# Kernel optimization log

Measured on AMD Instinct MI355X. Metric: run time of the kernel, lower is better.

## Reference

```python
import jax, jax.numpy as jnp
import numpy as np
from jax import lax

EPS = 1e-8
SLOPE = 0.2

def _modconv(x, wv, W, b, sW, sB, demodulate, pad):
    # StyleGAN2 modulated conv, expressed in the equivalent fused form:
    # scale input by per-sample style s, shared-weight conv, then demodulate output.
    s = wv @ sW.T + sB                                   # [B, Cin]
    y = lax.conv_general_dilated(
        x * s[:, :, None, None], W, (1, 1), [(pad, pad), (pad, pad)],
        dimension_numbers=("NCHW", "OIHW", "NCHW"))      # [B, Cout, H, W]
    if demodulate:
        # d[b,o] = 1/sqrt(sum_{i,k,k} (W[o,i,k,k]*s[b,i])^2 + eps)
        d = lax.rsqrt(jnp.einsum("oihw,bi->bo", W * W, s * s) + EPS)
        y = y * d[:, :, None, None]
    return y + b[None, :, None, None]

def _up2(x):
    B, C, H, W = x.shape
    # matches torch F.interpolate(scale_factor=2, mode='bilinear', align_corners=False)
    return jax.image.resize(x, (B, C, 2 * H, 2 * W), method="bilinear")

def setup_inputs() -> dict:
    B, CIN, COUT, NZ, H = 8, 512, 512, 512, 32
    key = jax.random.key(0)
    ks = jax.random.split(key, 20)
    wscale3 = 1.0 / np.sqrt(CIN * 9)   # kaiming-ish equalized-lr scale baked into weights
    wscale1 = 1.0 / np.sqrt(COUT)
    sscale = 1.0 / np.sqrt(NZ)
    return {
        "maps": jax.random.normal(ks[0], (B, CIN, H, H), jnp.float32),
        "w": jax.random.normal(ks[1], (B, NZ), jnp.float32),
        "rgb": jax.random.normal(ks[2], (B, 3, H, H), jnp.float32),
        "noise0": jax.random.normal(ks[3], (B, 1, 2 * H, 2 * H), jnp.float32),
        "noise1": jax.random.normal(ks[4], (B, 1, 2 * H, 2 * H), jnp.float32),
        "w0": jax.random.normal(ks[5], (COUT, CIN, 3, 3), jnp.float32) * wscale3,
        "b0": jnp.zeros((COUT,), jnp.float32),
        "sW0": jax.random.normal(ks[6], (CIN, NZ), jnp.float32) * sscale,
        "sB0": jnp.ones((CIN,), jnp.float32),
        "ns0": jax.random.normal(ks[7], (COUT,), jnp.float32) * 0.1,
        "w1": jax.random.normal(ks[8], (COUT, COUT, 3, 3), jnp.float32) * wscale3,
        "b1": jnp.zeros((COUT,), jnp.float32),
        "sW1": jax.random.normal(ks[9], (COUT, NZ), jnp.float32) * sscale,
        "sB1": jnp.ones((COUT,), jnp.float32),
        "ns1": jax.random.normal(ks[10], (COUT,), jnp.float32) * 0.1,
        "rgbW": jax.random.normal(ks[11], (3, COUT, 1, 1), jnp.float32) * wscale1,
        "rgbB": jnp.zeros((3,), jnp.float32),
        "rgbSW": jax.random.normal(ks[12], (COUT, NZ), jnp.float32) * sscale,
        "rgbSB": jnp.ones((COUT,), jnp.float32),
    }

def reference(maps, w, rgb, noise0, noise1,
              w0, b0, sW0, sB0, ns0,
              w1, b1, sW1, sB1, ns1,
              rgbW, rgbB, rgbSW, rgbSB):
    rgb = _up2(rgb)
    x = _up2(maps)
    # layer 0: modulated conv 3x3 + noise + leakyrelu
    x = _modconv(x, w, w0, b0, sW0, sB0, True, 1)
    x = x + ns0[None, :, None, None] * noise0
    x = jnp.where(x >= 0, x, SLOPE * x)
    # layer 1
    x = _modconv(x, w, w1, b1, sW1, sB1, True, 1)
    x = x + ns1[None, :, None, None] * noise1
    x = jnp.where(x >= 0, x, SLOPE * x)
    # to_rgb: modulated 1x1 conv, no demodulation
    rgb_out = rgb + _modconv(x, w, rgbW, rgbB, rgbSW, rgbSB, False, 0)
    return (rgb_out, x)
```

## Files before the change

kernel.cpp:

```cpp
#include <hip/hip_runtime.h>

typedef unsigned short u16;
typedef short bf16x8 __attribute__((ext_vector_type(8)));
typedef float f32x4 __attribute__((ext_vector_type(4)));
typedef u16 u16x4 __attribute__((ext_vector_type(4)));
typedef u16 u16x8 __attribute__((ext_vector_type(8)));
typedef unsigned u32x4 __attribute__((ext_vector_type(4)));

__device__ __forceinline__ float b2f(u16 v) {
  union { unsigned u; float f; } x; x.u = ((unsigned)v) << 16; return x.f;
}
__device__ __forceinline__ u16 f2b(float f) {
  unsigned u = __float_as_uint(f);
  unsigned r = (u + 0x7FFFu + ((u >> 16) & 1u)) >> 16;
  return (u16)r;
}
__device__ __forceinline__ float rin(const void* p, size_t i, int bf) {
  return bf ? b2f(((const u16*)p)[i]) : ((const float*)p)[i];
}
__device__ __forceinline__ void async16(const void* g, void* l) {
  __builtin_amdgcn_global_load_lds((const __attribute__((address_space(1))) unsigned*)g,
                                   (__attribute__((address_space(3))) unsigned*)l, 16, 0, 0);
}
__device__ __forceinline__ int detect_bf(const unsigned* __restrict__ w0raw, int tid, int* shflag) {
  if (tid < 64) {
    const unsigned lo = w0raw[tid] & 0xFFFFu;
    const unsigned e = (lo >> 7) & 0xFFu;
    const unsigned long long bad = __ballot(e < 100u || e > 126u);
    if (tid == 0) *shflag = (bad == 0ull) ? 1 : 0;
  }
  __syncthreads();
  return *shflag;
}

__global__ void styleall_kernel(const void* __restrict__ w,
                                const void* __restrict__ sW0, const void* __restrict__ sB0,
                                const void* __restrict__ sW1, const void* __restrict__ sB1,
                                const void* __restrict__ sWR, const void* __restrict__ sBR,
                                float* __restrict__ s0, float* __restrict__ s1,
                                float* __restrict__ sR, const unsigned* __restrict__ w0raw) {
  __shared__ int shflag;
  const int tid = threadIdx.x;
  const int bf = detect_bf(w0raw, tid, &shflag);
  const int mat = blockIdx.z, b = blockIdx.y, oc = blockIdx.x;
  const void* sW = (mat == 0) ? sW0 : ((mat == 1) ? sW1 : sWR);
  const void* sB = (mat == 0) ? sB0 : ((mat == 1) ? sB1 : sBR);
  float* out = (mat == 0) ? s0 : ((mat == 1) ? s1 : sR);
  const int i = oc * 64 + (tid >> 2), q = tid & 3;
  float acc = 0.f;
  if (bf) {
    const u16* rp = (const u16*)sW + (size_t)i * 512 + q * 128;
    const u16* wp = (const u16*)w + b * 512 + q * 128;
    for (int z = 0; z < 128; z += 8) {
      u16x8 a = *(const u16x8*)(rp + z), c = *(const u16x8*)(wp + z);
#pragma unroll
      for (int j = 0; j < 8; ++j) acc += b2f(a[j]) * b2f(c[j]);
    }
  } else {
    const float* rp = (const float*)sW + (size_t)i * 512 + q * 128;
    const float* wp = (const float*)w + b * 512 + q * 128;
    for (int z = 0; z < 128; z += 4) {
      f32x4 a = *(const f32x4*)(rp + z), c = *(const f32x4*)(wp + z);
#pragma unroll
      for (int j = 0; j < 4; ++j) acc += a[j] * c[j];
    }
  }
  acc += __shfl_xor(acc, 1, 64);
  acc += __shfl_xor(acc, 2, 64);
  if (q == 0) out[b * 512 + i] = acc + rin(sB, i, bf);
}

__global__ void demod_kernel(const void* __restrict__ W0, const void* __restrict__ W1,
                             const float* __restrict__ s0, const float* __restrict__ s1,
                             float* __restrict__ dm0, float* __restrict__ dm1,
                             u16* __restrict__ Wp0, u16* __restrict__ Wp1,
                             const unsigned* __restrict__ w0raw) {
  __shared__ int shflag;
  __shared__ float wl[4608];
  __shared__ float wsq[512];
  const int tid = threadIdx.x, lane = tid & 63, wv = tid >> 6;
  const int bf = detect_bf(w0raw, tid, &shflag);
  const int o = blockIdx.x, layer = blockIdx.y;
  const void* W = layer ? W1 : W0;
  const float* s = layer ? s1 : s0;
  float* d = layer ? dm1 : dm0;
  u16* Wp = layer ? Wp1 : Wp0;

  if (bf) {
    const u16* src = (const u16*)W + (size_t)o * 4608;
    for (int e = tid; e < 576; e += 256) {
      u16x8 v = *(const u16x8*)(src + e * 8);
#pragma unroll
      for (int j = 0; j < 8; ++j) wl[e * 8 + j] = b2f(v[j]);
    }
  } else {
    const float* src = (const float*)W + (size_t)o * 4608;
    for (int e = tid; e < 1152; e += 256) {
      f32x4 v = *(const f32x4*)(src + e * 4);
#pragma unroll
      for (int j = 0; j < 4; ++j) wl[e * 4 + j] = v[j];
    }
  }
  __syncthreads();
  for (int i = tid; i < 512; i += 256) {
    float ss = 0.f;
#pragma unroll
    for (int t = 0; t < 9; ++t) {
      const float f = wl[i * 9 + t];
      ss += f * f;
      Wp[t * 262144 + o * 512 + i] = f2b(f);
    }
    wsq[i] = ss;
  }
  __syncthreads();
#pragma unroll
  for (int bb = 0; bb < 2; ++bb) {
    const int b = wv * 2 + bb;
    float part = 0.f;
    for (int i = lane; i < 512; i += 64) { const float sv = s[b * 512 + i]; part += wsq[i] * sv * sv; }
#pragma unroll
    for (int st = 1; st < 64; st <<= 1) part += __shfl_xor(part, st, 64);
    if (lane == 0) d[b * 512 + o] = rsqrtf(part + 1e-8f);
  }
}

__global__ void prep_kernel(u16* __restrict__ actB, u32x4* __restrict__ zr, int NB) {
  const int id = blockIdx.x, tid = threadIdx.x;
  if (id < NB * 65) {
    const int bl = id / 65, sub = id - bl * 65;
    const int c = sub * 256 + tid;
    const int px = c >> 6, seg = c & 63;
    int oy, ox;
    if (px < 66)       { oy = 0;  ox = px; }
    else if (px < 132) { oy = 65; ox = px - 66; }
    else { const int e = px - 132; oy = 1 + (e >> 1); ox = (e & 1) * 65; }
    u32x4 z = {0, 0, 0, 0};
    *(u32x4*)&actB[((size_t)(bl * 4356) + oy * 66 + ox) * 512 + seg * 8] = z;
  } else {
    const int c = (id - NB * 65) * 256 + tid;
    if (c < 24832) { u32x4 z = {0, 0, 0, 0}; zr[c] = z; }
  }
}

__global__ void upsample_kernel(const void* __restrict__ maps, const float* __restrict__ s,
                                void* __restrict__ outb, int b_base,
                                const unsigned* __restrict__ w0raw) {
  __shared__ int shflag;
  __shared__ float it[32][2][33];
  const int tid = threadIdx.x;
  const int bf = detect_bf(w0raw, tid, &shflag);
  const size_t esz = bf ? 2 : 4;
  u16* xg = (u16*)((char*)outb + (98304 + (size_t)(b_base >> 2) * 8388608) * esz);
  const int oy = blockIdx.x;
  const int i0 = blockIdx.y * 32;
  const int bl = blockIdx.z;
  const int bg = b_base + bl;
  const int m = oy >> 1;
  int iy0, iy1; float wy0, wy1;
  if ((oy & 1) == 0) { iy0 = (m > 0) ? m - 1 : 0; iy1 = m; wy0 = 0.25f; wy1 = 0.75f; }
  else               { iy0 = m; iy1 = (m < 31) ? m + 1 : 31; wy0 = 0.75f; wy1 = 0.25f; }
#pragma unroll
  for (int k = 0; k < 8; ++k) {
    const int e = tid + k * 256;
    const int c = e >> 6, wsel = (e >> 5) & 1, x = e & 31;
    const int iy = wsel ? iy1 : iy0;
    it[c][wsel][x] = rin(maps, ((size_t)(bg * 512 + i0 + c) * 32 + iy) * 32 + x, bf);
  }
  __syncthreads();
#pragma unroll
  for (int k = 0; k < 8; ++k) {
    const int e = tid + k * 256;
    const int xx = e >> 5, c = e & 31;
    const int mx = xx >> 1;
    int ix0, ix1; float wx0, wx1;
    if ((xx & 1) == 0) { ix0 = (mx > 0) ? mx - 1 : 0; ix1 = mx; wx0 = 0.25f; wx1 = 0.75f; }
    else               { ix0 = mx; ix1 = (mx < 31) ? mx + 1 : 31; wx0 = 0.75f; wx1 = 0.25f; }
    const float r0 = wx0 * it[c][0][ix0] + wx1 * it[c][0][ix1];
    const float r1 = wx0 * it[c][1][ix0] + wx1 * it[c][1][ix1];
    const float v = (wy0 * r0 + wy1 * r1) * s[bg * 512 + i0 + c];
    xg[((size_t)(bl * 4096) + oy * 64 + xx) * 512 + i0 + c] = f2b(v);
  }
}

template <int L>
__global__ __launch_bounds__(512) void conv_kernel(
    void* __restrict__ outb, u16* __restrict__ actBp,
    const u16* __restrict__ Wp, const float* __restrict__ dmod,
    const void* __restrict__ bias, const void* __restrict__ nsc,
    const void* __restrict__ noise, const float* __restrict__ saux,
    const u16* __restrict__ zbuf, const void* __restrict__ rgbW,
    float* __restrict__ rgbacc, int b_base,
    const unsigned* __restrict__ w0raw) {
  __shared__ __attribute__((aligned(16))) u16 lds[65536];
  __shared__ float rgbWl[L == 1 ? 1536 : 4];
  __shared__ int shflag;
  const int tid = threadIdx.x, lane = tid & 63, w = tid >> 6;
  const int bf = detect_bf(w0raw, tid, &shflag);
  const size_t esz = bf ? 2 : 4;

  const int lin = blockIdx.x + (blockIdx.y << 4) + (blockIdx.z << 5);
  const int cpx = (int)(gridDim.z << 2);
  const int wg = (lin & 7) * cpx + (lin >> 3);
  const int bl = wg >> 5, rem = wg & 31;
  const int o0 = (rem >> 4) << 8, n0 = (rem & 15) << 8;
  const int bg = b_base + bl;
  const int wm = w >> 2, wn = w & 3;

  if constexpr (L == 1) {
    for (int e = tid; e < 1536; e += 512) rgbWl[e] = rin(rgbW, e, bf);
  }
  const u16* xg = (const u16*)((const char*)outb +
                  (98304 + (size_t)(b_base >> 2) * 8388608) * esz);

  const int q = lane >> 4, m15 = lane & 15;
  const int lro = m15 * 64 + ((q ^ (lane & 7)) * 8);
  const int srow8 = lane >> 3, schunk = (lane & 7) ^ srow8;
  const size_t aAst = (size_t)(o0 + srow8) * 512 + schunk * 8;

  const int ka0 = (w < 4) ? (2 * w) : (16 + 2 * (w - 4));
  const int ka1 = ka0 + 8;
  const int kbe = (w & 3) * 8 + (w >> 2) * 2;
  const int kb0 = kbe, kb1 = kbe + 1, kb2 = kbe + 4, kb3 = kbe + 5;
  size_t pB[4]; int oyv[4], oxv[4];
  {
    const int kk4[4] = {kb0, kb1, kb2, kb3};
#pragma unroll
    for (int j = 0; j < 4; ++j) {
      const int p = n0 + kk4[j] * 8 + srow8;
      const int oy = p >> 6, ox = p & 63;
      oyv[j] = oy; oxv[j] = ox;
      pB[j] = ((size_t)bl * 4356 + oy * 66 + ox) * 512 + schunk * 8;
    }
  }

#define STAGE_A(k_, aoff_) \
  async16(Wp + (aoff_) + (size_t)(k_) * 4096, &lds[nbb + (k_) * 512])
#define STAGE_B(j_, k_, sb_, ty1_, tx1_, ko_) do {                                   \
    if constexpr (L == 0) {                                                          \
      const int iy_ = oyv[j_] + (ty1_), ix_ = oxv[j_] + (tx1_);                      \
      const u16* s_ = (((unsigned)iy_ < 64u) & ((unsigned)ix_ < 64u))                \
        ? (xg + ((size_t)((bl << 12) + (iy_ << 6) + ix_) * 512 + (ko_) + schunk * 8))\
        : (zbuf + schunk * 8);                                                       \
      async16(s_, &lds[nbb + 16384 + (k_) * 512]);                                   \
    } else {                                                                         \
      async16(actBp + pB[j_] + (size_t)(sb_), &lds[nbb + 16384 + (k_) * 512]);       \
    } } while (0)

  f32x4 acc[8][4] = {};
  {
    const int nbb = 0;
    const size_t aoff = aAst;
    STAGE_A(ka0, aoff); STAGE_A(ka0 + 1, aoff);
    STAGE_A(ka1, aoff); STAGE_A(ka1 + 1, aoff);
    STAGE_B(0, kb0, 0, -1, -1, 0);
    STAGE_B(1, kb1, 0, -1, -1, 0);
    STAGE_B(2, kb2, 0, -1, -1, 0);
    STAGE_B(3, kb3, 0, -1, -1, 0);
  }
  asm volatile("s_waitcnt vmcnt(0)" ::: "memory");
  __builtin_amdgcn_s_barrier();

  bf16x8 afr[4][2], bfA[2][2], bfB[2][2];
#pragma unroll 1
  for (int s = 0; s < 72; ++s) {
    const int db = s & 1;
    const int dbb = db << 15, nbb = dbb ^ 32768;
    const int s1 = s + 1, ok = (s1 < 72);
    const int tn = s1 >> 3, kon = (s1 & 7) << 6;
    const int tyn = (tn * 11) >> 5, txn = tn - tyn * 3;
    const size_t aoffn = (size_t)tn * 262144 + kon + aAst;
    const int sbn = (tyn * 66 + txn) * 512 + kon;
    const int ty1 = tyn - 1, tx1 = txn - 1;
    const int abase = dbb + wm * 8192;
    const int bbase = dbb + 16384 + wn * 4096;

#pragma unroll
    for (int mi = 0; mi < 4; ++mi) {
      afr[mi][0] = *(const bf16x8*)&lds[abase + mi * 1024 + lro];
      afr[mi][1] = *(const bf16x8*)&lds[abase + mi * 1024 + (lro ^ 32)];
    }
#pragma unroll
    for (int ni = 0; ni < 2; ++ni) {
      bfA[ni][0] = *(const bf16x8*)&lds[bbase + ni * 1024 + lro];
      bfA[ni][1] = *(const bf16x8*)&lds[bbase + ni * 1024 + (lro ^ 32)];
    }
    if (ok) { STAGE_A(ka0, aoffn); STAGE_A(ka0 + 1, aoffn); }
    __builtin_amdgcn_s_setprio(1);
#pragma unroll
    for (int mi = 0; mi < 4; ++mi)
#pragma unroll
      for (int ni = 0; ni < 2; ++ni)
#pragma unroll
        for (int kk = 0; kk < 2; ++kk)
          acc[mi][ni] = __builtin_amdgcn_mfma_f32_16x16x32_bf16(
              afr[mi][kk], bfA[ni][kk], acc[mi][ni], 0, 0, 0);
    __builtin_amdgcn_s_setprio(0);
    if (ok) { asm volatile("s_waitcnt vmcnt(4)" ::: "memory"); }
    else    { asm volatile("s_waitcnt vmcnt(2)" ::: "memory"); }
    __builtin_amdgcn_s_barrier();

#pragma unroll
    for (int ni = 0; ni < 2; ++ni) {
      bfB[ni][0] = *(const bf16x8*)&lds[bbase + 2048 + ni * 1024 + lro];
      bfB[ni][1] = *(const bf16x8*)&lds[bbase + 2048 + ni * 1024 + (lro ^ 32)];
    }
    if (ok) { STAGE_B(0, kb0, sbn, ty1, tx1, kon); STAGE_B(1, kb1, sbn, ty1, tx1, kon); }
    __builtin_amdgcn_s_setprio(1);
#pragma unroll
    for (int mi = 0; mi < 4; ++mi)
#pragma unroll
      for (int ni = 0; ni < 2; ++ni)
#pragma unroll
        for (int kk = 0; kk < 2; ++kk)
          acc[mi][2 + ni] = __builtin_amdgcn_mfma_f32_16x16x32_bf16(
              afr[mi][kk], bfB[ni][kk], acc[mi][2 + ni], 0, 0, 0);
    __builtin_amdgcn_s_setprio(0);
    if (ok) { asm volatile("s_waitcnt vmcnt(4)" ::: "memory"); }
    else    { asm volatile("s_waitcnt vmcnt(0)" ::: "memory"); }
    __builtin_amdgcn_s_barrier();

#pragma unroll
    for (int mi = 0; mi < 4; ++mi) {
      afr[mi][0] = *(const bf16x8*)&lds[abase + 4096 + mi * 1024 + lro];
      afr[mi][1] = *(const bf16x8*)&lds[abase + 4096 + mi * 1024 + (lro ^ 32)];
    }
    if (ok) { STAGE_B(2, kb2, sbn, ty1, tx1, kon); STAGE_B(3, kb3, sbn, ty1, tx1, kon); }
    __builtin_amdgcn_s_setprio(1);
#pragma unroll
    for (int mi = 0; mi < 4; ++mi)
#pragma unroll
      for (int ni = 0; ni < 2; ++ni)
#pragma unroll
        for (int kk = 0; kk < 2; ++kk)
          acc[4 + mi][ni] = __builtin_amdgcn_mfma_f32_16x16x32_bf16(
              afr[mi][kk], bfA[ni][kk], acc[4 + mi][ni], 0, 0, 0);
    __builtin_amdgcn_s_setprio(0);

    if (ok) { STAGE_A(ka1, aoffn); STAGE_A(ka1 + 1, aoffn); }
    __builtin_amdgcn_s_setprio(1);
#pragma unroll
    for (int mi = 0; mi < 4; ++mi)
#pragma unroll
      for (int ni = 0; ni < 2; ++ni)
#pragma unroll
        for (int kk = 0; kk < 2; ++kk)
          acc[4 + mi][2 + ni] = __builtin_amdgcn_mfma_f32_16x16x32_bf16(
              afr[mi][kk], bfB[ni][kk], acc[4 + mi][2 + ni], 0, 0, 0);
    __builtin_amdgcn_s_setprio(0);
    asm volatile("s_waitcnt vmcnt(4)" ::: "memory");
    __builtin_amdgcn_s_barrier();
  }
#undef STAGE_A
#undef STAGE_B

  if constexpr (L == 0) {
#pragma unroll
    for (int ai = 0; ai < 8; ++ai) {
      const int o = o0 + wm * 128 + ai * 16 + q * 4;
      const f32x4 dv = *(const f32x4*)&dmod[bg * 512 + o];
      const f32x4 sv = *(const f32x4*)&saux[bg * 512 + o];
      float bv[4], nv[4];
#pragma unroll
      for (int r = 0; r < 4; ++r) { bv[r] = rin(bias, o + r, bf); nv[r] = rin(nsc, o + r, bf); }
#pragma unroll
      for (int bj = 0; bj < 4; ++bj) {
        const int p = n0 + wn * 64 + bj * 16 + m15;
        const float np = rin(noise, (size_t)bg * 4096 + p, bf);
        u16x4 pack;
#pragma unroll
        for (int r = 0; r < 4; ++r) {
          float v = acc[ai][bj][r] * dv[r] + bv[r] + nv[r] * np;
          v = (v >= 0.f) ? v : 0.2f * v;
          pack[r] = f2b(v * sv[r]);
        }
        const int oy = p >> 6, ox = p & 63;
        *(u16x4*)&actBp[((size_t)(bl * 4356) + (oy + 1) * 66 + (ox + 1)) * 512 + o] = pack;
      }
    }
  } else {
    char* xreg = (char*)outb + 98304 * esz;
    float racc[4][3] = {};
#pragma unroll
    for (int ai = 0; ai < 8; ++ai) {
      const int o = o0 + wm * 128 + ai * 16 + q * 4;
      const f32x4 dv = *(const f32x4*)&dmod[bg * 512 + o];
      const f32x4 srv = *(const f32x4*)&saux[bg * 512 + o];
      float bv[4], nv[4], w0l[4], w1l[4], w2l[4];
#pragma unroll
      for (int r = 0; r < 4; ++r) {
        bv[r] = rin(bias, o + r, bf); nv[r] = rin(nsc, o + r, bf);
        w0l[r] = rgbWl[o + r]; w1l[r] = rgbWl[512 + o + r]; w2l[r] = rgbWl[1024 + o + r];
      }
#pragma unroll
      for (int bj = 0; bj < 4; ++bj) {
        const int p = n0 + wn * 64 + bj * 16 + m15;
        const float np = rin(noise, (size_t)bg * 4096 + p, bf);
#pragma unroll
        for (int r = 0; r < 4; ++r) {
          float v = acc[ai][bj][r] * dv[r] + bv[r] + nv[r] * np;
          v = (v >= 0.f) ? v : 0.2f * v;
          const size_t xi = (size_t)(bg * 512 + o + r) * 4096 + p;
          if (bf) ((u16*)xreg)[xi] = f2b(v); else ((float*)xreg)[xi] = v;
          const float xr = v * srv[r];
          racc[bj][0] += w0l[r] * xr;
          racc[bj][1] += w1l[r] * xr;
          racc[bj][2] += w2l[r] * xr;
        }
      }
    }
#pragma unroll
    for (int bj = 0; bj < 4; ++bj) {
      const int p = n0 + wn * 64 + bj * 16 + m15;
#pragma unroll
      for (int c = 0; c < 3; ++c) {
        float t = racc[bj][c];
        t += __shfl_xor(t, 16, 64);
        t += __shfl_xor(t, 32, 64);
        if (lane < 16) atomicAdd(&rgbacc[(size_t)(bg * 3 + c) * 4096 + p], t);
      }
    }
  }
}

__global__ void rgbfin_kernel(const float* __restrict__ rgbacc, const void* __restrict__ rgbB,
                              const void* __restrict__ rgb, void* __restrict__ outb,
                              const unsigned* __restrict__ w0raw) {
  __shared__ int shflag;
  const int tid = threadIdx.x;
  const int bf = detect_bf(w0raw, tid, &shflag);
  const int g = blockIdx.x * 256 + tid;
  const int b = g >> 12, p = g & 4095;
  const int oy = p >> 6, ox = p & 63;
  const int m = oy >> 1; int iy0, iy1; float wy0, wy1;
  if ((oy & 1) == 0) { iy0 = (m > 0) ? m - 1 : 0; iy1 = m; wy0 = 0.25f; wy1 = 0.75f; }
  else               { iy0 = m; iy1 = (m < 31) ? m + 1 : 31; wy0 = 0.75f; wy1 = 0.25f; }
  const int mx = ox >> 1; int ix0, ix1; float wx0, wx1;
  if ((ox & 1) == 0) { ix0 = (mx > 0) ? mx - 1 : 0; ix1 = mx; wx0 = 0.25f; wx1 = 0.75f; }
  else               { ix0 = mx; ix1 = (mx < 31) ? mx + 1 : 31; wx0 = 0.75f; wx1 = 0.25f; }
#pragma unroll
  for (int c = 0; c < 3; ++c) {
    const size_t rb = (size_t)(b * 3 + c) * 1024;
    const float up = wy0 * (wx0 * rin(rgb, rb + iy0 * 32 + ix0, bf) + wx1 * rin(rgb, rb + iy0 * 32 + ix1, bf))
                   + wy1 * (wx0 * rin(rgb, rb + iy1 * 32 + ix0, bf) + wx1 * rin(rgb, rb + iy1 * 32 + ix1, bf));
    const float v = up + rin(rgbB, c, bf) + rgbacc[(size_t)(b * 3 + c) * 4096 + p];
    const size_t oi = ((size_t)(b * 3 + c) << 12) + p;
    if (bf) ((u16*)outb)[oi] = f2b(v); else ((float*)outb)[oi] = v;
  }
}


extern "C" void kernel_launch(void* const* d_in, const int* in_sizes, int n_in,
                              void* d_out, int out_size, void* d_ws, size_t ws_size,
                              hipStream_t stream) {
  const void* maps   = d_in[0];
  const void* wlat   = d_in[1];
  const void* rgb    = d_in[2];
  const void* noise0 = d_in[3];
  const void* noise1 = d_in[4];
  const void* w0     = d_in[5];
  const void* b0     = d_in[6];
  const void* sW0    = d_in[7];
  const void* sB0    = d_in[8];
  const void* ns0    = d_in[9];
  const void* w1     = d_in[10];
  const void* b1     = d_in[11];
  const void* sW1    = d_in[12];
  const void* sB1    = d_in[13];
  const void* ns1    = d_in[14];
  const void* rgbW   = d_in[15];
  const void* rgbB   = d_in[16];
  const void* rgbSW  = d_in[17];
  const void* rgbSB  = d_in[18];
  const unsigned* w0raw = (const unsigned*)w0;

  char* ws = (char*)d_ws;
  float* s0     = (float*)(ws + 1024);
  float* s1     = (float*)(ws + 17408);
  float* sR     = (float*)(ws + 33792);
  float* dm0    = (float*)(ws + 50176);
  float* dm1    = (float*)(ws + 66560);
  u16*   zbuf   = (u16*)(ws + 82944);
  float* rgbacc = (float*)(ws + 87040);
  u16*   Wp0    = (u16*)(ws + 480256);
  u16*   Wp1    = (u16*)(ws + 5198848);
  u16*   actB   = (u16*)(ws + 9917440);

  const bool full = ws_size >= (size_t)(9917440 + 35684352);
  const int NB = full ? 8 : 4;

  styleall_kernel<<<dim3(8, 8, 3), 256, 0, stream>>>(wlat, sW0, sB0, sW1, sB1, rgbSW, rgbSB,
                                                     s0, s1, sR, w0raw);
  demod_kernel<<<dim3(512, 2), 256, 0, stream>>>(w0, w1, s0, s1, dm0, dm1, Wp0, Wp1, w0raw);
  prep_kernel<<<NB * 65 + 97, 256, 0, stream>>>(actB, (u32x4*)zbuf, NB);

  for (int pass = 0; pass < 8 / NB; ++pass) {
    const int b_base = pass * NB;
    upsample_kernel<<<dim3(64, 16, NB), 256, 0, stream>>>(maps, s0, d_out, b_base, w0raw);
    conv_kernel<0><<<dim3(16, 2, NB), 512, 0, stream>>>(d_out, actB, Wp0, dm0,
        b0, ns0, noise0, s1, zbuf, nullptr, nullptr, b_base, w0raw);
    conv_kernel<1><<<dim3(16, 2, NB), 512, 0, stream>>>(d_out, actB, Wp1, dm1,
        b1, ns1, noise1, sR, zbuf, rgbW, rgbacc, b_base, w0raw);
  }
  rgbfin_kernel<<<128, 256, 0, stream>>>(rgbacc, rgbB, rgb, d_out, w0raw);
}
```

Before: 452.0 us.

## Restructure conv main loop addressing, add barriers, occupancy hint, swizzle upsample grid

Precomputes per-tap B source pointers and A offsets once per filter tap and advances them incrementally, replacing per-iteration index math with XOR-toggled LDS base registers. Adds extra workgroup barriers plus lgkmcnt waits and sched_barriers before each MFMA group so waves stay in lockstep and loads issue before compute. Sets launch_bounds minimum to two blocks per CU, and remaps upsample block indices so batch varies fastest. The added barriers can serialize waves, and the occupancy hint may cause register spills.

```diff
diff --git a/kernel.cpp b/kernel.cpp
--- a/kernel.cpp
+++ b/kernel.cpp
@@ -151,9 +151,13 @@
   const int bf = detect_bf(w0raw, tid, &shflag);
   const size_t esz = bf ? 2 : 4;
   u16* xg = (u16*)((char*)outb + (98304 + (size_t)(b_base >> 2) * 8388608) * esz);
-  const int oy = blockIdx.x;
-  const int i0 = blockIdx.y * 32;
-  const int bl = blockIdx.z;
+  int oy, i0, bl;
+  if (gridDim.z == 8) {
+    const int id = blockIdx.x + (blockIdx.y << 6) + (blockIdx.z << 10);
+    bl = id & 7; const int r = id >> 3; oy = r & 63; i0 = (r >> 6) << 5;
+  } else {
+    oy = blockIdx.x; i0 = blockIdx.y << 5; bl = blockIdx.z;
+  }
   const int bg = b_base + bl;
   const int m = oy >> 1;
   int iy0, iy1; float wy0, wy1;
@@ -183,7 +187,7 @@
 }
 
 template <int L>
-__global__ __launch_bounds__(512) void conv_kernel(
+__global__ __launch_bounds__(512, 2) void conv_kernel(
     void* __restrict__ outb, u16* __restrict__ actBp,
     const u16* __restrict__ Wp, const float* __restrict__ dmod,
     const void* __restrict__ bias, const void* __restrict__ nsc,
@@ -221,7 +225,8 @@
   const int ka1 = ka0 + 8;
   const int kbe = (w & 3) * 8 + (w >> 2) * 2;
   const int kb0 = kbe, kb1 = kbe + 1, kb2 = kbe + 4, kb3 = kbe + 5;
-  size_t pB[4]; int oyv[4], oxv[4];
+  int oyv[4], oxv[4];
+  size_t pB[4];
   {
     const int kk4[4] = {kb0, kb1, kb2, kb3};
 #pragma unroll
@@ -233,58 +238,71 @@
     }
   }
 
-#define STAGE_A(k_, aoff_) \
-  async16(Wp + (aoff_) + (size_t)(k_) * 4096, &lds[nbb + (k_) * 512])
-#define STAGE_B(j_, k_, sb_, ty1_, tx1_, ko_) do {                                   \
-    if constexpr (L == 0) {                                                          \
-      const int iy_ = oyv[j_] + (ty1_), ix_ = oxv[j_] + (tx1_);                      \
-      const u16* s_ = (((unsigned)iy_ < 64u) & ((unsigned)ix_ < 64u))                \
-        ? (xg + ((size_t)((bl << 12) + (iy_ << 6) + ix_) * 512 + (ko_) + schunk * 8))\
-        : (zbuf + schunk * 8);                                                       \
-      async16(s_, &lds[nbb + 16384 + (k_) * 512]);                                   \
-    } else {                                                                         \
-      async16(actBp + pB[j_] + (size_t)(sb_), &lds[nbb + 16384 + (k_) * 512]);       \
-    } } while (0)
+  const u16* bBase[4];
+  int koff, aoffu;
+  auto setTap = [&](int tn_) {
+    const int ty_ = (tn_ * 11) >> 5, tx_ = tn_ - ty_ * 3;
+    koff = 0;
+    aoffu = tn_ * 262144;
+    if constexpr (L == 0) {
+#pragma unroll
+      for (int j = 0; j < 4; ++j) {
+        const int iy_ = oyv[j] + ty_ - 1, ix_ = oxv[j] + tx_ - 1;
+        bBase[j] = (((unsigned)iy_ < 64u) & ((unsigned)ix_ < 64u))
+          ? (xg + ((size_t)((bl << 12) + (iy_ << 6) + ix_) * 512 + schunk * 8))
+          : (zbuf + schunk * 8);
+      }
+    } else {
+      const int sb_ = (ty_ * 66 + tx_) * 512;
+#pragma unroll
+      for (int j = 0; j < 4; ++j) bBase[j] = actBp + pB[j] + sb_;
+    }
+  };
+
+#define STAGE_A(k_) \
+  async16(Wp + aAst + (size_t)aoffu + (size_t)(k_) * 4096, &lds[stb + (k_) * 512])
+#define STAGE_B(j_, k_) \
+  async16(bBase[j_] + koff, &lds[stb + 16384 + (k_) * 512])
 
   f32x4 acc[8][4] = {};
   {
-    const int nbb = 0;
-    const size_t aoff = aAst;
-    STAGE_A(ka0, aoff); STAGE_A(ka0 + 1, aoff);
-    STAGE_A(ka1, aoff); STAGE_A(ka1 + 1, aoff);
-    STAGE_B(0, kb0, 0, -1, -1, 0);
-    STAGE_B(1, kb1, 0, -1, -1, 0);
-    STAGE_B(2, kb2, 0, -1, -1, 0);
-    STAGE_B(3, kb3, 0, -1, -1, 0);
-  }
+    setTap(0);
+    const int stb = 0;
+    STAGE_A(ka0); STAGE_A(ka0 + 1);
+    STAGE_A(ka1); STAGE_A(ka1 + 1);
+    STAGE_B(0, kb0); STAGE_B(1, kb1);
+    STAGE_B(2, kb2); STAGE_B(3, kb3);
+  }
+  koff = 64; aoffu = 64;
   asm volatile("s_waitcnt vmcnt(0)" ::: "memory");
   __builtin_amdgcn_s_barrier();
+
+  int arA  = wm * 8192 + lro;
+  int arAx = wm * 8192 + (lro ^ 32);
+  int arB  = 16384 + wn * 4096 + lro;
+  int arBx = 16384 + wn * 4096 + (lro ^ 32);
+  int stb  = 32768;
 
   bf16x8 afr[4][2], bfA[2][2], bfB[2][2];
 #pragma unroll 1
   for (int s = 0; s < 72; ++s) {
-    const int db = s & 1;
-    const int dbb = db << 15, nbb = dbb ^ 32768;
     const int s1 = s + 1, ok = (s1 < 72);
-    const int tn = s1 >> 3, kon = (s1 & 7) << 6;
-    const int tyn = (tn * 11) >> 5, txn = tn - tyn * 3;
-    const size_t aoffn = (size_t)tn * 262144 + kon + aAst;
-    const int sbn = (tyn * 66 + txn) * 512 + kon;
-    const int ty1 = tyn - 1, tx1 = txn - 1;
-    const int abase = dbb + wm * 8192;
-    const int bbase = dbb + 16384 + wn * 4096;
+    if (ok && (s1 & 7) == 0) setTap(s1 >> 3);
 
 #pragma unroll
     for (int mi = 0; mi < 4; ++mi) {
-      afr[mi][0] = *(const bf16x8*)&lds[abase + mi * 1024 + lro];
-      afr[mi][1] = *(const bf16x8*)&lds[abase + mi * 1024 + (lro ^ 32)];
+      afr[mi][0] = *(const bf16x8*)&lds[arA + mi * 1024];
+      afr[mi][1] = *(const bf16x8*)&lds[arAx + mi * 1024];
     }
 #pragma unroll
     for (int ni = 0; ni < 2; ++ni) {
-      bfA[ni][0] = *(const bf16x8*)&lds[bbase + ni * 1024 + lro];
-      bfA[ni][1] = *(const bf16x8*)&lds[bbase + ni * 1024 + (lro ^ 32)];
-    }
-    if (ok) { STAGE_A(ka0, aoffn); STAGE_A(ka0 + 1, aoffn); }
+      bfA[ni][0] = *(const bf16x8*)&lds[arB + ni * 1024];
+      bfA[ni][1] = *(const bf16x8*)&lds[arBx + ni * 1024];
+    }
+    if (ok) { STAGE_A(ka0); STAGE_A(ka0 + 1); }
+    __builtin_amdgcn_s_barrier();
+    asm volatile("s_waitcnt lgkmcnt(0)" ::: "memory");
+    __builtin_amdgcn_sched_barrier(0);
     __builtin_amdgcn_s_setprio(1);
 #pragma unroll
     for (int mi = 0; mi < 4; ++mi)
@@ -301,10 +319,13 @@
 
 #pragma unroll
     for (int ni = 0; ni < 2; ++ni) {
-      bfB[ni][0] = *(const bf16x8*)&lds[bbase + 2048 + ni * 1024 + lro];
-      bfB[ni][1] = *(const bf16x8*)&lds[bbase + 2048 + ni * 1024 + (lro ^ 32)];
-    }
-    if (ok) { STAGE_B(0, kb0, sbn, ty1, tx1, kon); STAGE_B(1, kb1, sbn, ty1, tx1, kon); }
+      bfB[ni][0] = *(const bf16x8*)&lds[arB + 2048 + ni * 1024];
+      bfB[ni][1] = *(const bf16x8*)&lds[arBx + 2048 + ni * 1024];
+    }
+    if (ok) { STAGE_B(0, kb0); STAGE_B(1, kb1); }
+    __builtin_amdgcn_s_barrier();
+    asm volatile("s_waitcnt lgkmcnt(0)" ::: "memory");
+    __builtin_amdgcn_sched_barrier(0);
     __builtin_amdgcn_s_setprio(1);
 #pragma unroll
     for (int mi = 0; mi < 4; ++mi)
@@ -321,10 +342,13 @@
 
 #pragma unroll
     for (int mi = 0; mi < 4; ++mi) {
-      afr[mi][0] = *(const bf16x8*)&lds[abase + 4096 + mi * 1024 + lro];
-      afr[mi][1] = *(const bf16x8*)&lds[abase + 4096 + mi * 1024 + (lro ^ 32)];
-    }
-    if (ok) { STAGE_B(2, kb2, sbn, ty1, tx1, kon); STAGE_B(3, kb3, sbn, ty1, tx1, kon); }
+      afr[mi][0] = *(const bf16x8*)&lds[arA + 4096 + mi * 1024];
+      afr[mi][1] = *(const bf16x8*)&lds[arAx + 4096 + mi * 1024];
+    }
+    if (ok) { STAGE_B(2, kb2); STAGE_B(3, kb3); }
+    __builtin_amdgcn_s_barrier();
+    asm volatile("s_waitcnt lgkmcnt(0)" ::: "memory");
+    __builtin_amdgcn_sched_barrier(0);
     __builtin_amdgcn_s_setprio(1);
 #pragma unroll
     for (int mi = 0; mi < 4; ++mi)
@@ -336,7 +360,7 @@
               afr[mi][kk], bfA[ni][kk], acc[4 + mi][ni], 0, 0, 0);
     __builtin_amdgcn_s_setprio(0);
 
-    if (ok) { STAGE_A(ka1, aoffn); STAGE_A(ka1 + 1, aoffn); }
+    if (ok) { STAGE_A(ka1); STAGE_A(ka1 + 1); }
     __builtin_amdgcn_s_setprio(1);
 #pragma unroll
     for (int mi = 0; mi < 4; ++mi)
@@ -349,6 +373,9 @@
     __builtin_amdgcn_s_setprio(0);
     asm volatile("s_waitcnt vmcnt(4)" ::: "memory");
     __builtin_amdgcn_s_barrier();
+
+    arA ^= 32768; arAx ^= 32768; arB ^= 32768; arBx ^= 32768; stb ^= 32768;
+    koff += 64; aoffu += 64;
   }
 #undef STAGE_A
 #undef STAGE_B
```

Measured after the change: 451.0 us. About the same (-0.2%).
